# Performance work log

Hardware: AMD Instinct MI355X
Metric: run time of the kernel (lower is better)

The kernel has to match this reference:

```python
import jax, jax.numpy as jnp
import numpy as np

B, T, D = 8, 2048, 512
F = 512          # filters (== D due to residual add)
K = 7            # kernel_size
H = 128          # hidden_dim of kernel generator (hard-coded in source)
LN_EPS = 1e-3    # keras LayerNormalization default epsilon


def setup_inputs() -> dict:
    key = jax.random.key(0)
    ks = jax.random.split(key, 8)
    x = jax.random.normal(ks[0], (B, T, D), dtype=jnp.float32)
    # kernel generator: Dense(D->H, relu) then Dense(H->K*F)
    W1 = jax.random.normal(ks[1], (D, H), dtype=jnp.float32) * (1.0 / np.sqrt(D))
    b1 = jnp.zeros((H,), dtype=jnp.float32)
    W2 = jax.random.normal(ks[2], (H, K * F), dtype=jnp.float32) * (1.0 / np.sqrt(H))
    b2 = jnp.zeros((K * F,), dtype=jnp.float32)
    # LayerNorm params
    gamma = jnp.ones((F,), dtype=jnp.float32)
    beta = jnp.zeros((F,), dtype=jnp.float32)
    return {"x": x, "W1": W1, "b1": b1, "W2": W2, "b2": b2,
            "gamma": gamma, "beta": beta}


def _dynamic_conv_block(x, W1, b1, W2, b2, gamma, beta):
    # per-token dynamic kernels: [B, T, K, F]
    h = jax.nn.relu(jnp.einsum("btd,dh->bth", x, W1) + b1)
    kernels = (jnp.einsum("bth,hf->btf", h, W2) + b2).reshape(B, T, K, F)
    # extract sliding-window patches (same padding): [B, T, K, D]
    pad = K // 2
    xp = jnp.pad(x, ((0, 0), (pad, pad), (0, 0)))
    patches = jnp.stack([xp[:, i:i + T, :] for i in range(K)], axis=2)
    # per-token conv: contract over window K and input channels D
    conv_out = jnp.einsum("btkd,btkf->btf", patches, kernels)
    # residual + LayerNorm + relu (dropout is identity at inference)
    y = conv_out + x
    mu = jnp.mean(y, axis=-1, keepdims=True)
    var = jnp.mean(jnp.square(y - mu), axis=-1, keepdims=True)
    y = (y - mu) * jax.lax.rsqrt(var + LN_EPS) * gamma + beta
    return jax.nn.relu(y)


def reference(x, W1, b1, W2, b2, gamma, beta):
    return _dynamic_conv_block(x, W1, b1, W2, b2, gamma, beta)
```

## Files before the change

### kernel.cpp

```cpp
#include <hip/hip_runtime.h>

#define NT 2048
#define ND 512
#define NH 128
#define NKW 7
#define KP 960
#define NTOK 16384

typedef float f32x4 __attribute__((ext_vector_type(4)));
typedef __bf16 bf16x8 __attribute__((ext_vector_type(8)));
typedef unsigned short u16;
typedef unsigned int u32;
typedef u16 u16x8 __attribute__((ext_vector_type(8)));

__device__ __forceinline__ u16 f2bf(float f){
  u32 u = __builtin_bit_cast(u32, f);
  return (u16)((u + 0x7fffu + ((u>>16)&1u)) >> 16);
}
__device__ __forceinline__ float bf2f(u16 s){
  u32 u = ((u32)s)<<16;
  return __builtin_bit_cast(float, u);
}
__device__ __forceinline__ bf16x8 pack8(const float4& a, const float4& b){
  u16x8 u;
  u[0]=f2bf(a.x); u[1]=f2bf(a.y); u[2]=f2bf(a.z); u[3]=f2bf(a.w);
  u[4]=f2bf(b.x); u[5]=f2bf(b.y); u[6]=f2bf(b.z); u[7]=f2bf(b.w);
  return __builtin_bit_cast(bf16x8, u);
}
__device__ __forceinline__ void store16_lds(void* p, const u16 u[8]){
  u32 d0 = (u32)u[0] | ((u32)u[1]<<16);
  u32 d1 = (u32)u[2] | ((u32)u[3]<<16);
  u32 d2 = (u32)u[4] | ((u32)u[5]<<16);
  u32 d3 = (u32)u[6] | ((u32)u[7]<<16);
  int4 vv; vv.x=(int)d0; vv.y=(int)d1; vv.z=(int)d2; vv.w=(int)d3;
  *(int4*)p = vv;
}

__global__ __launch_bounds__(256) void prep_kernel(
    const float* __restrict__ W1, const float* __restrict__ W2,
    const float* __restrict__ b2, u16* __restrict__ W1T, u16* __restrict__ B2T)
{
  __shared__ float T[64][65];
  const int b = blockIdx.x, tid = threadIdx.x;
  if (b < 16){
    const int d0 = (b>>1)*64, h0 = (b&1)*64;
    #pragma unroll
    for (int r=0;r<16;++r){
      int idx=r*256+tid; int dl=idx>>6, hl=idx&63;
      T[dl][hl] = W1[(size_t)(d0+dl)*NH + h0+hl];
    }
    __syncthreads();
    #pragma unroll
    for (int r=0;r<16;++r){
      int idx=r*256+tid; int hl=idx>>6, dl=idx&63;
      W1T[(size_t)(h0+hl)*ND + d0+dl] = f2bf(T[dl][hl]);
    }
  } else if (b < 128){
    const int bb = b-16;
    const int h0 = (bb&1)*64, c0 = (bb>>1)*64;
    #pragma unroll
    for (int r=0;r<16;++r){
      int idx=r*256+tid; int hl=idx>>6, cl=idx&63;
      T[hl][cl] = W2[(size_t)(h0+hl)*(NKW*ND) + c0+cl];
    }
    __syncthreads();
    #pragma unroll
    for (int r=0;r<16;++r){
      int idx=r*256+tid; int cl=idx>>6, hl=idx&63;
      int c = c0+cl; int n = c & (ND-1), k = c >> 9;
      B2T[(size_t)n*KP + k*NH + h0+hl] = f2bf(T[hl][cl]);
    }
  } else {
    const int bb = b-128;
    #pragma unroll
    for (int r=0;r<16;++r){
      int idx = bb*4096 + r*256 + tid;
      int n = idx>>6, j = idx&63;
      B2T[(size_t)n*KP + 896 + j] = (j<NKW)? f2bf(b2[(size_t)j*ND+n]) : (u16)0;
    }
  }
}

__global__ __launch_bounds__(512,2) void fused_kernel(
    const float* __restrict__ x, const u16* __restrict__ W1T,
    const float* __restrict__ b1, const u16* __restrict__ B2T,
    const float* __restrict__ gamma, const float* __restrict__ beta,
    float* __restrict__ out)
{
  __shared__ __align__(16) u16 xb_lds[64*512];
  __shared__ __align__(16) u16 h_lds[64*128];
  __shared__ __align__(16) u16 At[2][64*64];
  __shared__ float rs_lds[70];
  __shared__ float s_lds[64][8];
  __shared__ float red_s[64][8], red_q[64][8];
  __shared__ float mu_lds[64], rstd_lds[64];

  const int tid = threadIdx.x, w = tid>>6, l = tid&63;
  const int m_base = blockIdx.x*64;

  {
    const int r = tid>>3, slot = tid&7;
    const float4* p = (const float4*)(x + (size_t)(m_base+r)*ND + slot*64);
    float s = 0.f;
    #pragma unroll
    for (int i=0;i<8;++i){
      float4 a = p[2*i], b2v = p[2*i+1];
      s += (a.x+a.y)+(a.z+a.w) + (b2v.x+b2v.y)+(b2v.z+b2v.w);
      u16 u[8] = {f2bf(a.x),f2bf(a.y),f2bf(a.z),f2bf(a.w),
                  f2bf(b2v.x),f2bf(b2v.y),f2bf(b2v.z),f2bf(b2v.w)};
      int byte = r*1024 + ((slot*128 + i*16) ^ ((r&7)<<4));
      store16_lds((char*)xb_lds + byte, u);
    }
    s += __shfl_xor(s,1); s += __shfl_xor(s,2); s += __shfl_xor(s,4);
    if (slot==0) rs_lds[3+r] = s;
    if (l < 8 && w < 6){
      int j = (w<3)? w : w+64;
      int tg2 = m_base + j - 3;
      float s2 = 0.f;
      if (tg2 >= 0 && tg2 < NTOK){
        const float4* p2 = (const float4*)(x + (size_t)tg2*ND + l*64);
        #pragma unroll
        for (int i=0;i<16;++i){ float4 v = p2[i]; s2 += (v.x+v.y)+(v.z+v.w); }
      }
      s2 += __shfl_xor(s2,1); s2 += __shfl_xor(s2,2); s2 += __shfl_xor(s2,4);
      if (l==0) rs_lds[j] = s2;
    }
  }
  __syncthreads();
  {
    int rr = tid>>3, k = tid&7;
    float v = 0.f;
    if (k < NKW){
      int ti = (m_base+rr) & (NT-1);
      int idx = ti + k - 3;
      if (idx >= 0 && idx < NT) v = rs_lds[rr+k];
    }
    s_lds[rr][k] = v;
  }

  {
    const int wm = w>>2, wn = w&3;
    f32x4 acc1[2][2] = {};
    const u16* bbase = W1T + (size_t)(wn*32 + (l&15))*ND + (l>>4)*8;
    #pragma unroll
    for (int kc=0;kc<16;++kc){
      bf16x8 af[2], bfr[2];
      #pragma unroll
      for (int mi=0;mi<2;++mi){
        int rr = wm*32 + mi*16 + (l&15);
        int byte = rr*1024 + ((kc*64 + (l>>4)*16) ^ ((rr&7)<<4));
        af[mi] = *(const bf16x8*)((const char*)xb_lds + byte);
      }
      #pragma unroll
      for (int ni=0;ni<2;++ni)
        bfr[ni] = *(const bf16x8*)(bbase + (size_t)ni*16*ND + kc*32);
      #pragma unroll
      for (int mi=0;mi<2;++mi)
        #pragma unroll
        for (int ni=0;ni<2;++ni)
          acc1[mi][ni] = __builtin_amdgcn_mfma_f32_16x16x32_bf16(af[mi], bfr[ni], acc1[mi][ni],0,0,0);
    }
    #pragma unroll
    for (int ni=0;ni<2;++ni){
      int col = wn*32 + ni*16 + (l&15);
      float bias = b1[col];
      #pragma unroll
      for (int mi=0;mi<2;++mi){
        #pragma unroll
        for (int r=0;r<4;++r){
          int row = wm*32 + mi*16 + (l>>4)*4 + r;
          float v = fmaxf(acc1[mi][ni][r] + bias, 0.f);
          int byte = row*256 + ((2*col) ^ ((row&7)<<4));
          *(u16*)((char*)h_lds + byte) = f2bf(v);
        }
      }
    }
  }
  __syncthreads();

  f32x4 acc[4][4] = {};
  bf16x8 bufA[2][4], bufB[2][4];
  const int row = tid>>3, slot = tid&7;

  auto loadB = [&](int kc, bf16x8 (*bf)[4]){
    #pragma unroll
    for (int kk=0;kk<2;++kk)
      #pragma unroll
      for (int ni=0;ni<4;++ni){
        int rowB = w*64 + ni*16 + (l&15);
        bf[kk][ni] = *(const bf16x8*)((const char*)B2T + (size_t)rowB*(KP*2) + kc*128 + kk*64 + (l>>4)*16);
      }
  };
  auto stageA = [&](u16* dst, int kc2){
    u16 u[8];
    if (kc2 < 14){
      float sv = s_lds[row][kc2>>1];
      const char* src = (const char*)h_lds + row*256 + (((kc2&1)*128 + slot*16) ^ ((row&7)<<4));
      u16x8 hv = *(const u16x8*)src;
      #pragma unroll
      for (int j=0;j<8;++j) u[j] = f2bf(bf2f(hv[j])*sv);
    } else {
      #pragma unroll
      for (int j=0;j<8;++j){
        int e2 = slot*8+j;
        u[j] = (e2<NKW)? f2bf(s_lds[row][e2]) : (u16)0;
      }
    }
    int byte = row*128 + ((slot*16) ^ ((row&7)<<4));
    store16_lds((char*)dst + byte, u);
  };

  loadB(0, bufA);
  stageA(At[0], 0);
  __syncthreads();

  #pragma unroll
  for (int kc=0;kc<15;++kc){
    bf16x8 (*bc)[4] = (kc&1)? bufB : bufA;
    bf16x8 (*bn)[4] = (kc&1)? bufA : bufB;
    if (kc<14){
      loadB(kc+1, bn);
      __builtin_amdgcn_sched_barrier(0);
    }
    const char* curA = (const char*)At[kc&1];
    #pragma unroll
    for (int kk=0;kk<2;++kk){
      bf16x8 af[4];
      #pragma unroll
      for (int mi=0;mi<4;++mi){
        int r2 = mi*16 + (l&15);
        int byte = r2*128 + (((kk*64)+((l>>4)*16)) ^ ((r2&7)<<4));
        af[mi] = *(const bf16x8*)(curA + byte);
      }
      #pragma unroll
      for (int mi=0;mi<4;++mi)
        #pragma unroll
        for (int ni=0;ni<4;++ni)
          acc[mi][ni] = __builtin_amdgcn_mfma_f32_16x16x32_bf16(af[mi], bc[kk][ni], acc[mi][ni],0,0,0);
    }
    if (kc<14){
      stageA(At[(kc&1)^1], kc+1);
      __syncthreads();
    }
  }

  #pragma unroll
  for (int mi=0;mi<4;++mi){
    #pragma unroll
    for (int r=0;r<4;++r){
      int m = mi*16 + (l>>4)*4 + r;
      int tg = m_base + m;
      float ps=0.f, pq=0.f;
      #pragma unroll
      for (int ni=0;ni<4;++ni){
        int n = w*64 + ni*16 + (l&15);
        float v = acc[mi][ni][r] + x[(size_t)tg*ND + n];
        acc[mi][ni][r] = v;
        ps += v; pq += v*v;
      }
      #pragma unroll
      for (int msk=1; msk<16; msk<<=1){ ps += __shfl_xor(ps,msk); pq += __shfl_xor(pq,msk); }
      if ((l&15)==0){ red_s[m][w]=ps; red_q[m][w]=pq; }
    }
  }
  __syncthreads();
  if (tid < 64){
    float ssum=0.f, sq=0.f;
    #pragma unroll
    for (int ww=0; ww<8; ++ww){ ssum += red_s[tid][ww]; sq += red_q[tid][ww]; }
    float mu = ssum * (1.0f/ND);
    float var = sq*(1.0f/ND) - mu*mu;
    mu_lds[tid] = mu;
    rstd_lds[tid] = rsqrtf(var + 1e-3f);
  }
  __syncthreads();
  float gv[4], bv[4];
  #pragma unroll
  for (int ni=0;ni<4;++ni){
    int n = w*64 + ni*16 + (l&15);
    gv[ni] = gamma[n]; bv[ni] = beta[n];
  }
  #pragma unroll
  for (int mi=0;mi<4;++mi){
    #pragma unroll
    for (int r=0;r<4;++r){
      int m = mi*16 + (l>>4)*4 + r;
      int tg = m_base + m;
      float mu = mu_lds[m], rstd = rstd_lds[m];
      #pragma unroll
      for (int ni=0;ni<4;++ni){
        int n = w*64 + ni*16 + (l&15);
        float v = (acc[mi][ni][r]-mu)*rstd*gv[ni] + bv[ni];
        out[(size_t)tg*ND + n] = fmaxf(v, 0.f);
      }
    }
  }
}

extern "C" void kernel_launch(void* const* d_in, const int* in_sizes, int n_in,
                              void* d_out, int out_size, void* d_ws, size_t ws_size,
                              hipStream_t stream)
{
  (void)in_sizes; (void)n_in; (void)out_size; (void)ws_size;
  const float* x     = (const float*)d_in[0];
  const float* W1    = (const float*)d_in[1];
  const float* b1    = (const float*)d_in[2];
  const float* W2    = (const float*)d_in[3];
  const float* b2    = (const float*)d_in[4];
  const float* gamma = (const float*)d_in[5];
  const float* beta  = (const float*)d_in[6];
  float* out = (float*)d_out;

  char* ws = (char*)d_ws;
  u16* W1T = (u16*)(ws);
  u16* B2T = (u16*)(ws + 131072);

  prep_kernel<<<136, 256, 0, stream>>>(W1, W2, b2, W1T, B2T);
  fused_kernel<<<256, 512, 0, stream>>>(x, W1T, b1, B2T, gamma, beta, out);
}
```

Measured before the change: 144.2 us.

## Drop bf16 x LDS staging, fragment-ordered weights, overlapped staging/MFMA pipeline

The bf16 copy of x in LDS is removed; the first GEMM now reads x fragments straight from global memory and converts them in registers, which cuts LDS use. The weight prep kernel writes W1 and W2/b2 in MFMA-fragment-major order so B loads are contiguous per lane. The main loop is restructured as a ping-pong with staging of the next A tile issued before the MFMAs, using raw s_barrier plus lgkmcnt waits and s_setprio around the MFMA blocks. The risk is extra global traffic from the repeated x reads in the first GEMM.

```diff
diff --git a/kernel.cpp b/kernel.cpp
--- a/kernel.cpp
+++ b/kernel.cpp
@@ -4,7 +4,6 @@
 #define ND 512
 #define NH 128
 #define NKW 7
-#define KP 960
 #define NTOK 16384
 
 typedef float f32x4 __attribute__((ext_vector_type(4)));
@@ -27,7 +26,7 @@
   u[4]=f2bf(b.x); u[5]=f2bf(b.y); u[6]=f2bf(b.z); u[7]=f2bf(b.w);
   return __builtin_bit_cast(bf16x8, u);
 }
-__device__ __forceinline__ void store16_lds(void* p, const u16 u[8]){
+__device__ __forceinline__ void store16(void* p, const u16 u[8]){
   u32 d0 = (u32)u[0] | ((u32)u[1]<<16);
   u32 d1 = (u32)u[2] | ((u32)u[3]<<16);
   u32 d2 = (u32)u[4] | ((u32)u[5]<<16);
@@ -36,60 +35,41 @@
   *(int4*)p = vv;
 }
 
-__global__ __launch_bounds__(256) void prep_kernel(
+__global__ __launch_bounds__(256) void prep2_kernel(
     const float* __restrict__ W1, const float* __restrict__ W2,
-    const float* __restrict__ b2, u16* __restrict__ W1T, u16* __restrict__ B2T)
+    const float* __restrict__ b2, u16* __restrict__ W1F, u16* __restrict__ B3)
 {
-  __shared__ float T[64][65];
-  const int b = blockIdx.x, tid = threadIdx.x;
-  if (b < 16){
-    const int d0 = (b>>1)*64, h0 = (b&1)*64;
-    #pragma unroll
-    for (int r=0;r<16;++r){
-      int idx=r*256+tid; int dl=idx>>6, hl=idx&63;
-      T[dl][hl] = W1[(size_t)(d0+dl)*NH + h0+hl];
-    }
-    __syncthreads();
-    #pragma unroll
-    for (int r=0;r<16;++r){
-      int idx=r*256+tid; int hl=idx>>6, dl=idx&63;
-      W1T[(size_t)(h0+hl)*ND + d0+dl] = f2bf(T[dl][hl]);
-    }
-  } else if (b < 128){
-    const int bb = b-16;
-    const int h0 = (bb&1)*64, c0 = (bb>>1)*64;
-    #pragma unroll
-    for (int r=0;r<16;++r){
-      int idx=r*256+tid; int hl=idx>>6, cl=idx&63;
-      T[hl][cl] = W2[(size_t)(h0+hl)*(NKW*ND) + c0+cl];
-    }
-    __syncthreads();
-    #pragma unroll
-    for (int r=0;r<16;++r){
-      int idx=r*256+tid; int cl=idx>>6, hl=idx&63;
-      int c = c0+cl; int n = c & (ND-1), k = c >> 9;
-      B2T[(size_t)n*KP + k*NH + h0+hl] = f2bf(T[hl][cl]);
-    }
+  int f = blockIdx.x*256 + threadIdx.x;
+  u16 u[8];
+  if (f < 8192){
+    int n = f & 127, sk = f >> 7, kb = sk*8;
+    #pragma unroll
+    for (int j=0;j<8;++j) u[j] = f2bf(W1[(size_t)(kb+j)*NH + n]);
+    store16(W1F + (size_t)f*8, u);
   } else {
-    const int bb = b-128;
-    #pragma unroll
-    for (int r=0;r<16;++r){
-      int idx = bb*4096 + r*256 + tid;
-      int n = idx>>6, j = idx&63;
-      B2T[(size_t)n*KP + 896 + j] = (j<NKW)? f2bf(b2[(size_t)j*ND+n]) : (u16)0;
-    }
+    int g = f - 8192;
+    int n = g & 511, sc = g >> 9, kb = sc*8;
+    if (kb < 896){
+      int kwin = kb >> 7, h = kb & 127;
+      #pragma unroll
+      for (int j=0;j<8;++j) u[j] = f2bf(W2[(size_t)(h+j)*(NKW*ND) + kwin*ND + n]);
+    } else {
+      int jb = kb - 896;
+      #pragma unroll
+      for (int j=0;j<8;++j){ int jj = jb+j; u[j] = (jj<NKW)? f2bf(b2[(size_t)jj*ND + n]) : (u16)0; }
+    }
+    store16(B3 + (size_t)g*8, u);
   }
 }
 
 __global__ __launch_bounds__(512,2) void fused_kernel(
-    const float* __restrict__ x, const u16* __restrict__ W1T,
-    const float* __restrict__ b1, const u16* __restrict__ B2T,
+    const float* __restrict__ x, const u16* __restrict__ W1F,
+    const float* __restrict__ b1, const u16* __restrict__ B3,
     const float* __restrict__ gamma, const float* __restrict__ beta,
     float* __restrict__ out)
 {
-  __shared__ __align__(16) u16 xb_lds[64*512];
-  __shared__ __align__(16) u16 h_lds[64*128];
-  __shared__ __align__(16) u16 At[2][64*64];
+  __shared__ __align__(16) u16 h_lds[2*64*64];
+  __shared__ __align__(16) u16 At0[64*64], At1[64*64];
   __shared__ float rs_lds[70];
   __shared__ float s_lds[64][8];
   __shared__ float red_s[64][8], red_q[64][8];
@@ -98,33 +78,28 @@
   const int tid = threadIdx.x, w = tid>>6, l = tid&63;
   const int m_base = blockIdx.x*64;
 
-  {
-    const int r = tid>>3, slot = tid&7;
-    const float4* p = (const float4*)(x + (size_t)(m_base+r)*ND + slot*64);
-    float s = 0.f;
-    #pragma unroll
-    for (int i=0;i<8;++i){
-      float4 a = p[2*i], b2v = p[2*i+1];
-      s += (a.x+a.y)+(a.z+a.w) + (b2v.x+b2v.y)+(b2v.z+b2v.w);
-      u16 u[8] = {f2bf(a.x),f2bf(a.y),f2bf(a.z),f2bf(a.w),
-                  f2bf(b2v.x),f2bf(b2v.y),f2bf(b2v.z),f2bf(b2v.w)};
-      int byte = r*1024 + ((slot*128 + i*16) ^ ((r&7)<<4));
-      store16_lds((char*)xb_lds + byte, u);
-    }
+  #pragma unroll
+  for (int r=0;r<8;++r){
+    int row = w*8 + r;
+    const float4* pr = (const float4*)(x + (size_t)(m_base+row)*ND + l*8);
+    float4 a = pr[0], b = pr[1];
+    float s = (a.x+a.y)+(a.z+a.w)+((b.x+b.y)+(b.z+b.w));
     s += __shfl_xor(s,1); s += __shfl_xor(s,2); s += __shfl_xor(s,4);
-    if (slot==0) rs_lds[3+r] = s;
-    if (l < 8 && w < 6){
-      int j = (w<3)? w : w+64;
-      int tg2 = m_base + j - 3;
-      float s2 = 0.f;
-      if (tg2 >= 0 && tg2 < NTOK){
-        const float4* p2 = (const float4*)(x + (size_t)tg2*ND + l*64);
-        #pragma unroll
-        for (int i=0;i<16;++i){ float4 v = p2[i]; s2 += (v.x+v.y)+(v.z+v.w); }
-      }
-      s2 += __shfl_xor(s2,1); s2 += __shfl_xor(s2,2); s2 += __shfl_xor(s2,4);
-      if (l==0) rs_lds[j] = s2;
-    }
+    s += __shfl_xor(s,8); s += __shfl_xor(s,16); s += __shfl_xor(s,32);
+    if (l==0) rs_lds[3+row] = s;
+  }
+  if (w < 6){
+    int j = (w<3)? w : w+64;
+    int tg2 = m_base + j - 3;
+    float s2 = 0.f;
+    if (tg2 >= 0 && tg2 < NTOK){
+      const float4* p2 = (const float4*)(x + (size_t)tg2*ND + l*8);
+      float4 a = p2[0], b = p2[1];
+      s2 = (a.x+a.y)+(a.z+a.w)+((b.x+b.y)+(b.z+b.w));
+    }
+    s2 += __shfl_xor(s2,1); s2 += __shfl_xor(s2,2); s2 += __shfl_xor(s2,4);
+    s2 += __shfl_xor(s2,8); s2 += __shfl_xor(s2,16); s2 += __shfl_xor(s2,32);
+    if (l==0) rs_lds[j] = s2;
   }
   __syncthreads();
   {
@@ -141,19 +116,20 @@
   {
     const int wm = w>>2, wn = w&3;
     f32x4 acc1[2][2] = {};
-    const u16* bbase = W1T + (size_t)(wn*32 + (l&15))*ND + (l>>4)*8;
     #pragma unroll
     for (int kc=0;kc<16;++kc){
       bf16x8 af[2], bfr[2];
       #pragma unroll
       for (int mi=0;mi<2;++mi){
-        int rr = wm*32 + mi*16 + (l&15);
-        int byte = rr*1024 + ((kc*64 + (l>>4)*16) ^ ((rr&7)<<4));
-        af[mi] = *(const bf16x8*)((const char*)xb_lds + byte);
-      }
-      #pragma unroll
-      for (int ni=0;ni<2;++ni)
-        bfr[ni] = *(const bf16x8*)(bbase + (size_t)ni*16*ND + kc*32);
+        int row = wm*32 + mi*16 + (l&15);
+        const float4* px = (const float4*)(x + (size_t)(m_base+row)*ND + kc*32 + (l>>4)*8);
+        af[mi] = pack8(px[0], px[1]);
+      }
+      #pragma unroll
+      for (int ni=0;ni<2;++ni){
+        int n = wn*32 + ni*16 + (l&15);
+        bfr[ni] = *(const bf16x8*)(W1F + ((size_t)(kc*4 + (l>>4))*128 + n)*8);
+      }
       #pragma unroll
       for (int mi=0;mi<2;++mi)
         #pragma unroll
@@ -164,38 +140,38 @@
     for (int ni=0;ni<2;++ni){
       int col = wn*32 + ni*16 + (l&15);
       float bias = b1[col];
-      #pragma unroll
-      for (int mi=0;mi<2;++mi){
+      int half = col>>6, cc = col&63;
+      #pragma unroll
+      for (int mi=0;mi<2;++mi)
         #pragma unroll
         for (int r=0;r<4;++r){
           int row = wm*32 + mi*16 + (l>>4)*4 + r;
           float v = fmaxf(acc1[mi][ni][r] + bias, 0.f);
-          int byte = row*256 + ((2*col) ^ ((row&7)<<4));
+          int byte = half*8192 + row*128 + ((cc*2) ^ ((row&7)<<4));
           *(u16*)((char*)h_lds + byte) = f2bf(v);
         }
-      }
     }
   }
   __syncthreads();
 
   f32x4 acc[4][4] = {};
-  bf16x8 bufA[2][4], bufB[2][4];
-  const int row = tid>>3, slot = tid&7;
-
-  auto loadB = [&](int kc, bf16x8 (*bf)[4]){
+  bf16x8 bE[2][4], bO[2][4];
+  const int row3 = tid>>3, slot = tid&7;
+
+  auto loadB = [&](int c, bf16x8 (&bf)[2][4]){
     #pragma unroll
     for (int kk=0;kk<2;++kk)
       #pragma unroll
       for (int ni=0;ni<4;++ni){
         int rowB = w*64 + ni*16 + (l&15);
-        bf[kk][ni] = *(const bf16x8*)((const char*)B2T + (size_t)rowB*(KP*2) + kc*128 + kk*64 + (l>>4)*16);
+        bf[kk][ni] = *(const bf16x8*)(B3 + ((size_t)((c*2+kk)*4 + (l>>4))*512 + rowB)*8);
       }
   };
-  auto stageA = [&](u16* dst, int kc2){
+  auto stageA = [&](u16* dst, int c){
     u16 u[8];
-    if (kc2 < 14){
-      float sv = s_lds[row][kc2>>1];
-      const char* src = (const char*)h_lds + row*256 + (((kc2&1)*128 + slot*16) ^ ((row&7)<<4));
+    if (c < 14){
+      float sv = s_lds[row3][c>>1];
+      const char* src = (const char*)h_lds + (c&1)*8192 + row3*128 + ((slot*16) ^ ((row3&7)<<4));
       u16x8 hv = *(const u16x8*)src;
       #pragma unroll
       for (int j=0;j<8;++j) u[j] = f2bf(bf2f(hv[j])*sv);
@@ -203,26 +179,13 @@
       #pragma unroll
       for (int j=0;j<8;++j){
         int e2 = slot*8+j;
-        u[j] = (e2<NKW)? f2bf(s_lds[row][e2]) : (u16)0;
-      }
-    }
-    int byte = row*128 + ((slot*16) ^ ((row&7)<<4));
-    store16_lds((char*)dst + byte, u);
+        u[j] = (e2<NKW)? f2bf(s_lds[row3][e2]) : (u16)0;
+      }
+    }
+    store16((char*)dst + row3*128 + ((slot*16) ^ ((row3&7)<<4)), u);
   };
-
-  loadB(0, bufA);
-  stageA(At[0], 0);
-  __syncthreads();
-
-  #pragma unroll
-  for (int kc=0;kc<15;++kc){
-    bf16x8 (*bc)[4] = (kc&1)? bufB : bufA;
-    bf16x8 (*bn)[4] = (kc&1)? bufA : bufB;
-    if (kc<14){
-      loadB(kc+1, bn);
-      __builtin_amdgcn_sched_barrier(0);
-    }
-    const char* curA = (const char*)At[kc&1];
+  auto mfmaC = [&](const u16* A, bf16x8 (&b)[2][4]){
+    __builtin_amdgcn_s_setprio(1);
     #pragma unroll
     for (int kk=0;kk<2;++kk){
       bf16x8 af[4];
@@ -230,19 +193,37 @@
       for (int mi=0;mi<4;++mi){
         int r2 = mi*16 + (l&15);
         int byte = r2*128 + (((kk*64)+((l>>4)*16)) ^ ((r2&7)<<4));
-        af[mi] = *(const bf16x8*)(curA + byte);
+        af[mi] = *(const bf16x8*)((const char*)A + byte);
       }
       #pragma unroll
       for (int mi=0;mi<4;++mi)
         #pragma unroll
         for (int ni=0;ni<4;++ni)
-          acc[mi][ni] = __builtin_amdgcn_mfma_f32_16x16x32_bf16(af[mi], bc[kk][ni], acc[mi][ni],0,0,0);
-    }
-    if (kc<14){
-      stageA(At[(kc&1)^1], kc+1);
-      __syncthreads();
-    }
-  }
+          acc[mi][ni] = __builtin_amdgcn_mfma_f32_16x16x32_bf16(af[mi], b[kk][ni], acc[mi][ni],0,0,0);
+    }
+    __builtin_amdgcn_s_setprio(0);
+  };
+  #define SYNC() do{ __builtin_amdgcn_sched_barrier(0); \
+      asm volatile("s_waitcnt lgkmcnt(0)" ::: "memory"); \
+      __builtin_amdgcn_s_barrier(); \
+      __builtin_amdgcn_sched_barrier(0); }while(0)
+
+  loadB(0, bE);
+  stageA(At0, 0);
+  SYNC();
+  #pragma unroll
+  for (int t=0;t<7;++t){
+    loadB(2*t+1, bO);
+    stageA(At1, 2*t+1);
+    mfmaC(At0, bE);
+    SYNC();
+    loadB(2*t+2, bE);
+    stageA(At0, 2*t+2);
+    mfmaC(At1, bO);
+    SYNC();
+  }
+  mfmaC(At0, bE);
+  #undef SYNC
 
   #pragma unroll
   for (int mi=0;mi<4;++mi){
@@ -312,9 +293,9 @@
   float* out = (float*)d_out;
 
   char* ws = (char*)d_ws;
-  u16* W1T = (u16*)(ws);
-  u16* B2T = (u16*)(ws + 131072);
-
-  prep_kernel<<<136, 256, 0, stream>>>(W1, W2, b2, W1T, B2T);
-  fused_kernel<<<256, 512, 0, stream>>>(x, W1T, b1, B2T, gamma, beta, out);
-}
+  u16* W1F = (u16*)(ws);
+  u16* B3  = (u16*)(ws + 131072);
+
+  prep2_kernel<<<272, 256, 0, stream>>>(W1, W2, b2, W1F, B3);
+  fused_kernel<<<256, 512, 0, stream>>>(x, W1F, b1, B3, gamma, beta, out);
+}
```

After: 139.6 us. 1.03x faster.
